# Performance work log

Measured on AMD Instinct MI355X. Metric: run time of the kernel, lower is better.

Reference implementation:

```python
import jax, jax.numpy as jnp
import numpy as np


def _maxpool2x2(t):
    # t: [B, C, H, W] -> [B, C, H//2, W//2]
    b, c, h, w = t.shape
    return t.reshape(b, c, h // 2, 2, w // 2, 2).max(axis=(3, 5))


def setup_inputs() -> dict:
    key = jax.random.key(0)
    ks = jax.random.split(key, 6)
    B, C, H, W = 16, 64, 64, 64
    x = jax.random.normal(ks[0], (B, C, H, W), dtype=jnp.float32)
    # 1x1 conv weights (no bias), stored as [out_ch, in_ch]
    s = 0.05
    W_theta = jax.random.normal(ks[1], (C // 8, C), dtype=jnp.float32) * s
    W_phi = jax.random.normal(ks[2], (C // 8, C), dtype=jnp.float32) * s
    W_g = jax.random.normal(ks[3], (C // 2, C), dtype=jnp.float32) * s
    W_attn = jax.random.normal(ks[4], (C, C // 2), dtype=jnp.float32) * s
    sigma = jnp.ones((1,), dtype=jnp.float32) * 0.5  # nonzero so attn path matters
    return {"x": x, "W_theta": W_theta, "W_phi": W_phi, "W_g": W_g,
            "W_attn": W_attn, "sigma": sigma}


def reference(x, W_theta, W_phi, W_g, W_attn, sigma):
    B, C, H, W = x.shape
    N = H * W
    M = N // 4
    # 1x1 convs are channel matmuls
    theta = jnp.einsum('oc,bchw->bohw', W_theta, x).reshape(B, C // 8, N)      # [B, C/8, N]
    phi = _maxpool2x2(jnp.einsum('oc,bchw->bohw', W_phi, x)).reshape(B, C // 8, M)  # [B, C/8, M]
    attn = jax.nn.softmax(jnp.einsum('bkn,bkm->bnm', theta, phi), axis=-1)    # [B, N, M]
    g = _maxpool2x2(jnp.einsum('oc,bchw->bohw', W_g, x)).reshape(B, C // 2, M)  # [B, C/2, M]
    attn_g = jnp.einsum('bgm,bnm->bgn', g, attn).reshape(B, C // 2, H, W)      # [B, C/2, H, W]
    attn_g = jnp.einsum('oc,bchw->bohw', W_attn, attn_g)                        # [B, C, H, W]
    return x + sigma * attn_g
```

## Files before the change

### kernel.cpp

```cpp
#include <hip/hip_runtime.h>
#include <hip/hip_bf16.h>

#define CC 64
#define NN 4096
#define MM 1024

typedef __attribute__((ext_vector_type(4))) short s4b;
typedef __attribute__((ext_vector_type(4))) float float4v;

__device__ inline unsigned short f2bf(float f) {
    union { float f; unsigned u; } v; v.f = f;
    unsigned r = v.u + 0x7fff + ((v.u >> 16) & 1);
    return (unsigned short)(r >> 16);
}

__device__ inline float4v mfma16(s4b a, s4b b, float4v c) {
#if __has_builtin(__builtin_amdgcn_mfma_f32_16x16x16bf16_1k)
    return __builtin_amdgcn_mfma_f32_16x16x16bf16_1k(a, b, c, 0, 0, 0);
#else
    float4v d;
    asm volatile("v_mfma_f32_16x16x16_bf16 %0, %1, %2, %3"
                 : "=v"(d) : "v"(a), "v"(b), "v"(c));
    return d;
#endif
}

__global__ __launch_bounds__(256) void prep_kernel(
    const float* __restrict__ x,
    const float* __restrict__ Wth,
    const float* __restrict__ Wph,
    const float* __restrict__ Wg,
    unsigned short* __restrict__ thT,
    unsigned short* __restrict__ phiP,
    unsigned short* __restrict__ gP)
{
    __shared__ float wt[64 * 48];
    __shared__ float buf[128 * 49];

    const int tid  = threadIdx.x;
    const int b    = blockIdx.y;
    const int hp   = blockIdx.x;
    const int pix  = tid & 127;
    const int half = tid >> 7;

    for (int idx = tid; idx < 64 * 48; idx += 256) {
        const int c = idx / 48, j = idx % 48;
        float v;
        if (j < 8)       v = Wth[j * 64 + c];
        else if (j < 16) v = Wph[(j - 8) * 64 + c];
        else             v = Wg[(j - 16) * 64 + c];
        wt[c * 48 + j] = v;
    }
    __syncthreads();

    const int n = (2 * hp + (pix >> 6)) * 64 + (pix & 63);
    const float* xb = x + (size_t)b * CC * NN + (size_t)half * 32 * NN + n;

    float acc[48];
#pragma unroll
    for (int j = 0; j < 48; ++j) acc[j] = 0.f;

#pragma unroll
    for (int c0 = 0; c0 < 32; c0 += 16) {
        float xv[16];
#pragma unroll
        for (int u = 0; u < 16; ++u) xv[u] = xb[(size_t)(c0 + u) * NN];
#pragma unroll
        for (int u = 0; u < 16; ++u) {
            const float* wrow = &wt[(half * 32 + c0 + u) * 48];
#pragma unroll
            for (int j = 0; j < 48; ++j) acc[j] += wrow[j] * xv[u];
        }
    }

    if (half == 1) {
#pragma unroll
        for (int j = 0; j < 48; ++j) buf[pix * 49 + j] = acc[j];
    }
    __syncthreads();

    if (half == 0) {
#pragma unroll
        for (int j = 0; j < 48; ++j) acc[j] += buf[pix * 49 + j];
        union { unsigned short s[8]; uint4 v; } pk;
#pragma unroll
        for (int j = 0; j < 8; ++j) pk.s[j] = f2bf(acc[j] * 1.44269504f);
        *(uint4*)&thT[((size_t)b * NN + n) * 8] = pk.v;
#pragma unroll
        for (int j = 0; j < 40; ++j) buf[pix * 49 + j] = acc[8 + j];
    }
    __syncthreads();

    for (int idx = tid; idx < 1280; idx += 256) {
        const int pm = idx & 31;
        const int j  = idx >> 5;
        const int p00 = 2 * pm, p10 = 64 + 2 * pm;
        const float v = fmaxf(fmaxf(buf[p00 * 49 + j], buf[(p00 + 1) * 49 + j]),
                              fmaxf(buf[p10 * 49 + j], buf[(p10 + 1) * 49 + j]));
        const int m = hp * 32 + pm;
        if (j < 8) phiP[((size_t)b * MM + m) * 8 + j] = f2bf(v);
        else       gP[((size_t)b * 32 + (j - 8)) * MM + m] = f2bf(v);
    }
}

__global__ __launch_bounds__(256) void attn_mfma(
    const unsigned short* __restrict__ thT,
    const unsigned short* __restrict__ phiP,
    const unsigned short* __restrict__ gP,
    const float* __restrict__ x,
    const float* __restrict__ Wa,
    const float* __restrict__ sigma,
    float* __restrict__ out)
{
    constexpr int GP = 264;
    constexpr int OP = 36;

    __shared__ __align__(16) union {
        struct {
            unsigned short phi[256 * 8 + 16];
            unsigned short g[32 * GP];
        } m;
        float obar[64 * OP];
    } sh;
    __shared__ __align__(16) float wa_s[64 * 32];

    const int tid  = threadIdx.x;
    const int lane = tid & 63;
    const int wv   = tid >> 6;
    const int c15  = lane & 15;
    const int quad = lane >> 4;
    const int b    = blockIdx.y;
    const int n0   = blockIdx.x * 64;

    for (int i = tid; i < 2048; i += 256) wa_s[i] = Wa[i];

    s4b zero4 = {0, 0, 0, 0};
    s4b bth = zero4;
    if (quad < 2) {
        union { uint2 u; s4b s; } t;
        t.u = *(const uint2*)&thT[((size_t)b * NN + n0 + wv * 16 + c15) * 8 + quad * 4];
        bth = t.s;
    }

    float4v acc0 = {0.f, 0.f, 0.f, 0.f};
    float4v acc1 = {0.f, 0.f, 0.f, 0.f};
    float zacc = 0.f;

    for (int ch = 0; ch < 4; ++ch) {
        __syncthreads();
        *(uint4*)&sh.m.phi[tid * 8] =
            *(const uint4*)&phiP[((size_t)b * MM + ch * 256 + tid) * 8];
        if (tid < 2) {
            uint4 z4; z4.x = z4.y = z4.z = z4.w = 0u;
            *(uint4*)&sh.m.phi[256 * 8 + tid * 8] = z4;
        }
#pragma unroll
        for (int it = 0; it < 4; ++it) {
            const int idx = tid + 256 * it;
            const int row = idx >> 5, c32 = idx & 31;
            *(uint4*)&sh.m.g[row * GP + c32 * 8] =
                *(const uint4*)&gP[((size_t)b * 32 + row) * MM + ch * 256 + c32 * 8];
        }
        __syncthreads();

#pragma unroll 4
        for (int st = 0; st < 16; ++st) {
            const int kb = st * 16;

            union { uint2 u; s4b s; } ap;
            ap.u = *(const uint2*)&sh.m.phi[(kb + c15) * 8 + quad * 4];

            float4v cz = {0.f, 0.f, 0.f, 0.f};
            float4v sc = mfma16(ap.s, bth, cz);

            union { float f; unsigned u; } e0, e1, e2, e3;
            e0.f = __builtin_amdgcn_exp2f(sc[0]);
            e1.f = __builtin_amdgcn_exp2f(sc[1]);
            e2.f = __builtin_amdgcn_exp2f(sc[2]);
            e3.f = __builtin_amdgcn_exp2f(sc[3]);
            zacc += (e0.f + e1.f) + (e2.f + e3.f);
            union { uint2 u; s4b s; } pa;
            pa.u.x = __builtin_amdgcn_perm(e1.u, e0.u, 0x07060302u);
            pa.u.y = __builtin_amdgcn_perm(e3.u, e2.u, 0x07060302u);

            union { uint2 u; s4b s; } bg0, bg1;
            bg0.u = *(const uint2*)&sh.m.g[c15 * GP + kb + quad * 4];
            bg1.u = *(const uint2*)&sh.m.g[(16 + c15) * GP + kb + quad * 4];

            acc0 = mfma16(pa.s, bg0.s, acc0);
            acc1 = mfma16(pa.s, bg1.s, acc1);
        }
    }

    float z = zacc;
    z += __shfl_xor(z, 16, 64);
    z += __shfl_xor(z, 32, 64);
    const float rzq = __builtin_amdgcn_rcpf(z);

    __syncthreads();

#pragma unroll
    for (int r = 0; r < 4; ++r) {
        const float rz = __shfl(rzq, quad * 4 + r, 64);
        const int ql = wv * 16 + quad * 4 + r;
        sh.obar[ql * OP + c15]      = acc0[r] * rz;
        sh.obar[ql * OP + 16 + c15] = acc1[r] * rz;
    }
    __syncthreads();

    {
        const int q  = tid & 63;
        const int og = tid >> 6;
        float a[16];
#pragma unroll
        for (int i = 0; i < 16; ++i) a[i] = 0.f;
        const float4* ob4 = (const float4*)&sh.obar[q * OP];
        const float4* wa4 = (const float4*)wa_s;
#pragma unroll
        for (int g4 = 0; g4 < 8; ++g4) {
            const float4 ob = ob4[g4];
#pragma unroll
            for (int i = 0; i < 16; ++i) {
                const float4 w = wa4[(og * 16 + i) * 8 + g4];
                a[i] += w.x * ob.x + w.y * ob.y + w.z * ob.z + w.w * ob.w;
            }
        }
        const float sg = sigma[0];
#pragma unroll
        for (int i = 0; i < 16; ++i) {
            const size_t oi = ((size_t)b * CC + og * 16 + i) * NN + n0 + q;
            out[oi] = x[oi] + sg * a[i];
        }
    }
}

extern "C" void kernel_launch(void* const* d_in, const int* in_sizes, int n_in,
                              void* d_out, int out_size, void* d_ws, size_t ws_size,
                              hipStream_t stream) {
    const float* x      = (const float*)d_in[0];
    const float* W_th   = (const float*)d_in[1];
    const float* W_ph   = (const float*)d_in[2];
    const float* W_g    = (const float*)d_in[3];
    const float* W_attn = (const float*)d_in[4];
    const float* sigma  = (const float*)d_in[5];
    float* out = (float*)d_out;

    const int B = 16;
    unsigned short* thT  = (unsigned short*)d_ws;
    unsigned short* phiP = thT + (size_t)B * NN * 8;
    unsigned short* gP   = phiP + (size_t)B * MM * 8;

    prep_kernel<<<dim3(32, 16), 256, 0, stream>>>(x, W_th, W_ph, W_g,
                                                  thT, phiP, gP);
    attn_mfma<<<dim3(64, 16), 256, 0, stream>>>(thT, phiP, gP, x,
                                                W_attn, sigma, out);
}
```

Measured before the change: 115.7 us.

## Use 16x16x32 bf16 MFMA for PV and W_attn projection, permute phi layout

The PV accumulation now uses the 16x16x32 bf16 MFMA, consuming two score tiles per step. Phi rows are stored to LDS in a permuted order so each lane's exp outputs line up with the wider K fragment. The final W_attn 1x1 projection moves from scalar FP32 dot products over LDS to bf16 MFMA, with weights held as per-lane register fragments. This cuts LDS traffic and VALU work in the epilogue, at the cost of extra bf16 rounding on the attention output and the weights.

```diff
diff --git a/kernel.cpp b/kernel.cpp
--- a/kernel.cpp
+++ b/kernel.cpp
@@ -6,6 +6,7 @@
 #define MM 1024
 
 typedef __attribute__((ext_vector_type(4))) short s4b;
+typedef __attribute__((ext_vector_type(8))) short s8b;
 typedef __attribute__((ext_vector_type(4))) float float4v;
 
 __device__ inline unsigned short f2bf(float f) {
@@ -20,6 +21,17 @@
 #else
     float4v d;
     asm volatile("v_mfma_f32_16x16x16_bf16 %0, %1, %2, %3"
+                 : "=v"(d) : "v"(a), "v"(b), "v"(c));
+    return d;
+#endif
+}
+
+__device__ inline float4v mfma32(s8b a, s8b b, float4v c) {
+#if __has_builtin(__builtin_amdgcn_mfma_f32_16x16x32_bf16)
+    return __builtin_amdgcn_mfma_f32_16x16x32_bf16(a, b, c, 0, 0, 0);
+#else
+    float4v d;
+    asm volatile("v_mfma_f32_16x16x32_bf16 %0, %1, %2, %3"
                  : "=v"(d) : "v"(a), "v"(b), "v"(c));
     return d;
 #endif
@@ -113,16 +125,15 @@
     float* __restrict__ out)
 {
     constexpr int GP = 264;
-    constexpr int OP = 36;
+    constexpr int OBP = 40;
 
     __shared__ __align__(16) union {
         struct {
             unsigned short phi[256 * 8 + 16];
             unsigned short g[32 * GP];
         } m;
-        float obar[64 * OP];
+        unsigned short obb[64 * OBP];
     } sh;
-    __shared__ __align__(16) float wa_s[64 * 32];
 
     const int tid  = threadIdx.x;
     const int lane = tid & 63;
@@ -132,7 +143,16 @@
     const int b    = blockIdx.y;
     const int n0   = blockIdx.x * 64;
 
-    for (int i = tid; i < 2048; i += 256) wa_s[i] = Wa[i];
+    union { unsigned short s[8]; s8b v; } wfrag;
+    {
+        const float* wr = Wa + (wv * 16 + c15) * 32 + quad * 8;
+        const float4 w0 = *(const float4*)wr;
+        const float4 w1 = *(const float4*)(wr + 4);
+        wfrag.s[0] = f2bf(w0.x); wfrag.s[1] = f2bf(w0.y);
+        wfrag.s[2] = f2bf(w0.z); wfrag.s[3] = f2bf(w0.w);
+        wfrag.s[4] = f2bf(w1.x); wfrag.s[5] = f2bf(w1.y);
+        wfrag.s[6] = f2bf(w1.z); wfrag.s[7] = f2bf(w1.w);
+    }
 
     s4b zero4 = {0, 0, 0, 0};
     s4b bth = zero4;
@@ -148,11 +168,16 @@
 
     for (int ch = 0; ch < 4; ++ch) {
         __syncthreads();
-        *(uint4*)&sh.m.phi[tid * 8] =
-            *(const uint4*)&phiP[((size_t)b * MM + ch * 256 + tid) * 8];
-        if (tid < 2) {
-            uint4 z4; z4.x = z4.y = z4.z = z4.w = 0u;
-            *(uint4*)&sh.m.phi[256 * 8 + tid * 8] = z4;
+        {
+            const int r  = tid & 7;
+            const int q3 = (tid >> 3) & 3;
+            const int slot = (tid & ~31) | ((r >> 2) << 4) | (q3 << 2) | (r & 3);
+            *(uint4*)&sh.m.phi[slot * 8] =
+                *(const uint4*)&phiP[((size_t)b * MM + ch * 256 + tid) * 8];
+            if (tid < 2) {
+                uint4 z4; z4.x = z4.y = z4.z = z4.w = 0u;
+                *(uint4*)&sh.m.phi[256 * 8 + tid * 8] = z4;
+            }
         }
 #pragma unroll
         for (int it = 0; it < 4; ++it) {
@@ -163,32 +188,43 @@
         }
         __syncthreads();
 
-#pragma unroll 4
-        for (int st = 0; st < 16; ++st) {
-            const int kb = st * 16;
-
-            union { uint2 u; s4b s; } ap;
-            ap.u = *(const uint2*)&sh.m.phi[(kb + c15) * 8 + quad * 4];
+        const unsigned short* pA  = &sh.m.phi[c15 * 8 + quad * 4];
+        const unsigned short* pg0 = &sh.m.g[c15 * GP + quad * 8];
+        const unsigned short* pg1 = pg0 + 16 * GP;
+
+#pragma unroll
+        for (int g32 = 0; g32 < 8; ++g32) {
+            union { uint2 u; s4b s; } apA, apB;
+            apA.u = *(const uint2*)&pA[g32 * 256];
+            apB.u = *(const uint2*)&pA[g32 * 256 + 128];
 
             float4v cz = {0.f, 0.f, 0.f, 0.f};
-            float4v sc = mfma16(ap.s, bth, cz);
-
-            union { float f; unsigned u; } e0, e1, e2, e3;
-            e0.f = __builtin_amdgcn_exp2f(sc[0]);
-            e1.f = __builtin_amdgcn_exp2f(sc[1]);
-            e2.f = __builtin_amdgcn_exp2f(sc[2]);
-            e3.f = __builtin_amdgcn_exp2f(sc[3]);
-            zacc += (e0.f + e1.f) + (e2.f + e3.f);
-            union { uint2 u; s4b s; } pa;
-            pa.u.x = __builtin_amdgcn_perm(e1.u, e0.u, 0x07060302u);
-            pa.u.y = __builtin_amdgcn_perm(e3.u, e2.u, 0x07060302u);
-
-            union { uint2 u; s4b s; } bg0, bg1;
-            bg0.u = *(const uint2*)&sh.m.g[c15 * GP + kb + quad * 4];
-            bg1.u = *(const uint2*)&sh.m.g[(16 + c15) * GP + kb + quad * 4];
-
-            acc0 = mfma16(pa.s, bg0.s, acc0);
-            acc1 = mfma16(pa.s, bg1.s, acc1);
+            float4v scA = mfma16(apA.s, bth, cz);
+            float4v scB = mfma16(apB.s, bth, cz);
+
+            union { float f; unsigned u; } a0, a1, a2, a3, b0, b1, b2, b3;
+            a0.f = __builtin_amdgcn_exp2f(scA[0]);
+            a1.f = __builtin_amdgcn_exp2f(scA[1]);
+            a2.f = __builtin_amdgcn_exp2f(scA[2]);
+            a3.f = __builtin_amdgcn_exp2f(scA[3]);
+            b0.f = __builtin_amdgcn_exp2f(scB[0]);
+            b1.f = __builtin_amdgcn_exp2f(scB[1]);
+            b2.f = __builtin_amdgcn_exp2f(scB[2]);
+            b3.f = __builtin_amdgcn_exp2f(scB[3]);
+            zacc += ((a0.f + a1.f) + (a2.f + a3.f)) +
+                    ((b0.f + b1.f) + (b2.f + b3.f));
+            union { uint4 u; s8b s; } pa;
+            pa.u.x = __builtin_amdgcn_perm(a1.u, a0.u, 0x07060302u);
+            pa.u.y = __builtin_amdgcn_perm(a3.u, a2.u, 0x07060302u);
+            pa.u.z = __builtin_amdgcn_perm(b1.u, b0.u, 0x07060302u);
+            pa.u.w = __builtin_amdgcn_perm(b3.u, b2.u, 0x07060302u);
+
+            union { uint4 u; s8b s; } bg0, bg1;
+            bg0.u = *(const uint4*)&pg0[g32 * 32];
+            bg1.u = *(const uint4*)&pg1[g32 * 32];
+
+            acc0 = mfma32(pa.s, bg0.s, acc0);
+            acc1 = mfma32(pa.s, bg1.s, acc1);
         }
     }
 
@@ -203,33 +239,23 @@
     for (int r = 0; r < 4; ++r) {
         const float rz = __shfl(rzq, quad * 4 + r, 64);
         const int ql = wv * 16 + quad * 4 + r;
-        sh.obar[ql * OP + c15]      = acc0[r] * rz;
-        sh.obar[ql * OP + 16 + c15] = acc1[r] * rz;
-    }
-    __syncthreads();
-
-    {
-        const int q  = tid & 63;
-        const int og = tid >> 6;
-        float a[16];
-#pragma unroll
-        for (int i = 0; i < 16; ++i) a[i] = 0.f;
-        const float4* ob4 = (const float4*)&sh.obar[q * OP];
-        const float4* wa4 = (const float4*)wa_s;
-#pragma unroll
-        for (int g4 = 0; g4 < 8; ++g4) {
-            const float4 ob = ob4[g4];
-#pragma unroll
-            for (int i = 0; i < 16; ++i) {
-                const float4 w = wa4[(og * 16 + i) * 8 + g4];
-                a[i] += w.x * ob.x + w.y * ob.y + w.z * ob.z + w.w * ob.w;
-            }
-        }
-        const float sg = sigma[0];
-#pragma unroll
-        for (int i = 0; i < 16; ++i) {
-            const size_t oi = ((size_t)b * CC + og * 16 + i) * NN + n0 + q;
-            out[oi] = x[oi] + sg * a[i];
+        sh.obb[ql * OBP + c15]      = f2bf(acc0[r] * rz);
+        sh.obb[ql * OBP + 16 + c15] = f2bf(acc1[r] * rz);
+    }
+    __syncthreads();
+
+    const float sg = sigma[0];
+#pragma unroll
+    for (int t = 0; t < 4; ++t) {
+        union { uint4 u; s8b s; } bo;
+        bo.u = *(const uint4*)&sh.obb[(t * 16 + c15) * OBP + quad * 8];
+        float4v cz = {0.f, 0.f, 0.f, 0.f};
+        float4v oc = mfma32(wfrag.v, bo.s, cz);
+#pragma unroll
+        for (int r = 0; r < 4; ++r) {
+            const size_t oi = ((size_t)b * CC + wv * 16 + quad * 4 + r) * NN
+                              + n0 + t * 16 + c15;
+            out[oi] = x[oi] + sg * oc[r];
         }
     }
 }
```

Result: faster. 105.2 us (-9.1%).
